# Kernel optimization log

Measured on AMD Instinct MI355X. Metric: run time of the kernel, lower is better.

The kernel has to match this reference:

```python
import jax, jax.numpy as jnp
import numpy as np

D_MODEL = 256
D_FFN = 1024
N_LEVELS = 4
N_HEADS = 8
N_POINTS = 4
HEAD_DIM = D_MODEL // N_HEADS
SPATIAL = [(128, 128), (64, 64), (32, 32), (16, 16)]
LQ = sum(h * w for h, w in SPATIAL)  # 21760
B = 2


def setup_inputs() -> dict:
    key = jax.random.key(0)
    ks = jax.random.split(key, 24)

    def w(k, shape, s=0.02):
        return (jax.random.normal(k, shape) * s).astype(jnp.float32)

    HLP = N_HEADS * N_LEVELS * N_POINTS
    starts = np.cumsum([0] + [h * w_ for h, w_ in SPATIAL[:-1]])
    return {
        "src": jax.random.normal(ks[0], (B, LQ, D_MODEL), jnp.float32),
        "pos": 0.1 * jax.random.normal(ks[1], (B, LQ, D_MODEL), jnp.float32),
        "reference_points": jax.random.uniform(ks[2], (B, LQ, N_LEVELS, 2), jnp.float32),
        "W_off": w(ks[3], (D_MODEL, HLP * 2)),
        "b_off": w(ks[4], (HLP * 2,), 0.5),
        "W_attn": w(ks[5], (D_MODEL, HLP)),
        "b_attn": jnp.zeros((HLP,), jnp.float32),
        "W_val": w(ks[6], (D_MODEL, D_MODEL)),
        "b_val": jnp.zeros((D_MODEL,), jnp.float32),
        "W_out": w(ks[7], (D_MODEL, D_MODEL)),
        "b_out": jnp.zeros((D_MODEL,), jnp.float32),
        "ln1_g": jnp.ones((D_MODEL,), jnp.float32),
        "ln1_b": jnp.zeros((D_MODEL,), jnp.float32),
        "W1": w(ks[8], (D_MODEL, D_FFN)),
        "b1": jnp.zeros((D_FFN,), jnp.float32),
        "W2": w(ks[9], (D_FFN, D_MODEL)),
        "b2": jnp.zeros((D_MODEL,), jnp.float32),
        "ln2_g": jnp.ones((D_MODEL,), jnp.float32),
        "ln2_b": jnp.zeros((D_MODEL,), jnp.float32),
        "spatial_shapes": np.array(SPATIAL, np.int32),
        "level_start_index": np.array(starts, np.int32),
    }


def _layernorm(x, g, b):
    mu = x.mean(-1, keepdims=True)
    var = ((x - mu) ** 2).mean(-1, keepdims=True)
    return (x - mu) * jax.lax.rsqrt(var + 1e-5) * g + b


def _bilinear_sample(v, x, y, H, W):
    # v: [N, H, W, D]; x, y: [N, Lq, P] pixel coords (align_corners=False, zero pad)
    x0f = jnp.floor(x)
    y0f = jnp.floor(y)
    x0 = x0f.astype(jnp.int32)
    y0 = y0f.astype(jnp.int32)
    wx1 = x - x0f
    wy1 = y - y0f
    wx0 = 1.0 - wx1
    wy0 = 1.0 - wy1
    vf = v.reshape(v.shape[0], H * W, v.shape[-1])

    def gather(xi, yi, wt):
        valid = (xi >= 0) & (xi < W) & (yi >= 0) & (yi < H)
        idx = jnp.clip(yi, 0, H - 1) * W + jnp.clip(xi, 0, W - 1)
        g = jnp.take_along_axis(vf, idx.reshape(idx.shape[0], -1)[..., None], axis=1)
        g = g.reshape(*xi.shape, vf.shape[-1])
        return g * (wt * valid.astype(wt.dtype))[..., None]

    return (gather(x0, y0, wx0 * wy0) + gather(x0 + 1, y0, wx1 * wy0)
            + gather(x0, y0 + 1, wx0 * wy1) + gather(x0 + 1, y0 + 1, wx1 * wy1))


def _ms_deform_attn(query, src, reference_points, W_off, b_off, W_attn, b_attn,
                    W_val, b_val, W_out, b_out, spatial_shapes):
    Bq, Lq, _ = query.shape
    ss = np.asarray(spatial_shapes)
    value = (src @ W_val + b_val).reshape(Bq, Lq, N_HEADS, HEAD_DIM)
    off = (query @ W_off + b_off).reshape(Bq, Lq, N_HEADS, N_LEVELS, N_POINTS, 2)
    attn = (query @ W_attn + b_attn).reshape(Bq, Lq, N_HEADS, N_LEVELS * N_POINTS)
    attn = jax.nn.softmax(attn, axis=-1).reshape(Bq, Lq, N_HEADS, N_LEVELS, N_POINTS)
    # offset normalizer = (W, H) per level
    normalizer = jnp.asarray(ss[:, ::-1].astype(np.float32))  # [L, 2]
    loc = reference_points[:, :, None, :, None, :] + off / normalizer[None, None, None, :, None, :]
    # loc: [B, Lq, M, L, P, 2] normalized in [0,1]
    out = jnp.zeros((Bq, N_HEADS, Lq, HEAD_DIM), query.dtype)
    start = 0
    for lvl in range(N_LEVELS):
        H, W = int(ss[lvl, 0]), int(ss[lvl, 1])
        v = value[:, start:start + H * W]                                 # [B, HW, M, D]
        v = v.transpose(0, 2, 1, 3).reshape(Bq * N_HEADS, H, W, HEAD_DIM)
        l = loc[:, :, :, lvl]                                             # [B, Lq, M, P, 2]
        x = (l[..., 0] * W - 0.5).transpose(0, 2, 1, 3).reshape(Bq * N_HEADS, Lq, N_POINTS)
        y = (l[..., 1] * H - 0.5).transpose(0, 2, 1, 3).reshape(Bq * N_HEADS, Lq, N_POINTS)
        sampled = _bilinear_sample(v, x, y, H, W)                         # [BM, Lq, P, D]
        wgt = attn[:, :, :, lvl].transpose(0, 2, 1, 3).reshape(Bq * N_HEADS, Lq, N_POINTS)
        out = out + (sampled * wgt[..., None]).sum(2).reshape(Bq, N_HEADS, Lq, HEAD_DIM)
        start += H * W
    out = out.transpose(0, 2, 1, 3).reshape(Bq, Lq, D_MODEL)
    return out @ W_out + b_out


def reference(src, pos, reference_points, W_off, b_off, W_attn, b_attn, W_val, b_val,
              W_out, b_out, ln1_g, ln1_b, W1, b1, W2, b2, ln2_g, ln2_b,
              spatial_shapes, level_start_index):
    query = src + pos
    src2 = _ms_deform_attn(query, src, reference_points, W_off, b_off, W_attn, b_attn,
                           W_val, b_val, W_out, b_out, spatial_shapes)
    h = _layernorm(src + src2, ln1_g, ln1_b)
    ffn = jax.nn.relu(h @ W1 + b1) @ W2 + b2
    return _layernorm(h + ffn, ln2_g, ln2_b)
```

## Files before the change

kernel.cpp:

```cpp
#include <hip/hip_runtime.h>

typedef __bf16 bf16x8 __attribute__((ext_vector_type(8)));
typedef float f32x4 __attribute__((ext_vector_type(4)));

static constexpr int TOKS = 43520;
static constexpr int LQN  = 21760;

__device__ __forceinline__ unsigned short f2bf(float f) {
  union { float f; unsigned u; } v; v.f = f;
  return (unsigned short)((v.u + 0x7fffu + ((v.u >> 16) & 1u)) >> 16);
}
__device__ __forceinline__ float bf2f(unsigned short b) {
  union { unsigned u; float f; } v; v.u = ((unsigned)b) << 16; return v.f;
}

__global__ __launch_bounds__(256) void prewt_kernel(
    const float* __restrict__ src, const float* __restrict__ pos,
    unsigned short* __restrict__ srcb, unsigned short* __restrict__ qb,
    const float* __restrict__ W_val, const float* __restrict__ W_off,
    const float* __restrict__ W_attn, const float* __restrict__ W_out,
    const float* __restrict__ W1, const float* __restrict__ W2,
    const float* __restrict__ b_off, const float* __restrict__ b_attn,
    unsigned short* __restrict__ Wt_val, unsigned short* __restrict__ Wt_oa,
    unsigned short* __restrict__ Wt_out,
    unsigned short* __restrict__ Wt_1, unsigned short* __restrict__ Wt_2,
    float* __restrict__ b_oa) {
  const int bid = blockIdx.x;
  if (bid < 10880) {
    int i = bid * 256 + threadIdx.x;
    float4 s = ((const float4*)src)[i], p = ((const float4*)pos)[i];
    ((ushort4*)srcb)[i] = make_ushort4(f2bf(s.x), f2bf(s.y), f2bf(s.z), f2bf(s.w));
    ((ushort4*)qb)[i]   = make_ushort4(f2bf(s.x + p.x), f2bf(s.y + p.y),
                                       f2bf(s.z + p.z), f2bf(s.w + p.w));
    return;
  }
  int gid = (bid - 10880) * 256 + threadIdx.x;
  if (gid >= 754048) return;
  if (gid >= 753664) {
    int i = gid - 753664;
    b_oa[i] = (i < 256) ? b_off[i] : b_attn[i - 256];
    return;
  }
  const float* W; unsigned short* Wt; int idx, K, nsh;
  if (gid < 65536)       { W = W_val;  Wt = Wt_val;          idx = gid;          K = 256;  nsh = 8;  }
  else if (gid < 131072) { W = W_off;  Wt = Wt_oa;           idx = gid - 65536;  K = 256;  nsh = 8;  }
  else if (gid < 163840) { W = W_attn; Wt = Wt_oa + 65536;   idx = gid - 131072; K = 256;  nsh = 7;  }
  else if (gid < 229376) { W = W_out;  Wt = Wt_out;          idx = gid - 163840; K = 256;  nsh = 8;  }
  else if (gid < 491520) { W = W1;     Wt = Wt_1;            idx = gid - 229376; K = 256;  nsh = 10; }
  else                   { W = W2;     Wt = Wt_2;            idx = gid - 491520; K = 1024; nsh = 8;  }
  int k = idx >> nsh, n = idx & ((1 << nsh) - 1);
  Wt[n * K + k] = f2bf(W[idx]);
}

template <int K, int OUTOP>
__device__ __forceinline__ void gemm_body(unsigned short* __restrict__ As,
                                          unsigned short* __restrict__ Bs,
                                          const unsigned short* __restrict__ A,
                                          const unsigned short* __restrict__ Bt,
                                          const float* __restrict__ bias,
                                          const unsigned short* __restrict__ res,
                                          unsigned short* __restrict__ Cp,
                                          int N, int bm, int bn) {
  const int t = threadIdx.x;
  const int wave = t >> 6, lane = t & 63;
  const int wm = (wave & 1) << 6, wn = (wave >> 1) << 6;
  const int lr = lane & 15, lq = lane >> 4;
  const int row0 = t >> 2, cb0 = (t & 3) << 3;
  f32x4 acc[4][4] = {};
  const unsigned short* ga = A  + (size_t)(bm * 128 + row0) * K + cb0;
  const unsigned short* gb = Bt + (size_t)(bn * 128 + row0) * K + cb0;
  const size_t gs = (size_t)64 * K;
  uint4 pa0 = *(const uint4*)ga;
  uint4 pa1 = *(const uint4*)(ga + gs);
  uint4 pb0 = *(const uint4*)gb;
  uint4 pb1 = *(const uint4*)(gb + gs);
  int p = 0;
#pragma unroll 1
  for (int k0 = 0; k0 < K; k0 += 32) {
    unsigned short* Ab = As + p * 5120;
    unsigned short* Bb = Bs + p * 5120;
    *(uint4*)&Ab[row0 * 40 + cb0] = pa0;
    *(uint4*)&Ab[(row0 + 64) * 40 + cb0] = pa1;
    *(uint4*)&Bb[row0 * 40 + cb0] = pb0;
    *(uint4*)&Bb[(row0 + 64) * 40 + cb0] = pb1;
    __syncthreads();
    if (k0 + 32 < K) {
      pa0 = *(const uint4*)(ga + k0 + 32);
      pa1 = *(const uint4*)(ga + gs + k0 + 32);
      pb0 = *(const uint4*)(gb + k0 + 32);
      pb1 = *(const uint4*)(gb + gs + k0 + 32);
    }
    bf16x8 af[4], bfr[4];
#pragma unroll
    for (int i = 0; i < 4; i++) af[i] = *(const bf16x8*)&Ab[(wm + i * 16 + lr) * 40 + lq * 8];
#pragma unroll
    for (int j = 0; j < 4; j++) bfr[j] = *(const bf16x8*)&Bb[(wn + j * 16 + lr) * 40 + lq * 8];
#pragma unroll
    for (int i = 0; i < 4; i++)
#pragma unroll
      for (int j = 0; j < 4; j++)
        acc[i][j] = __builtin_amdgcn_mfma_f32_16x16x32_bf16(af[i], bfr[j], acc[i][j], 0, 0, 0);
    p ^= 1;
  }
  const int rb = bm * 128 + wm + lq * 4;
  const int cbase = bn * 128 + wn + lr;
#pragma unroll
  for (int j = 0; j < 4; j++) {
    const int col = cbase + j * 16;
    const float bv = bias[col];
#pragma unroll
    for (int i = 0; i < 4; i++) {
#pragma unroll
      for (int r = 0; r < 4; r++) {
        float v = acc[i][j][r] + bv;
        size_t o = (size_t)(rb + i * 16 + r) * N + col;
        if (OUTOP == 1) Cp[o] = f2bf(v);
        else if (OUTOP == 2) Cp[o] = f2bf(fmaxf(v, 0.f));
        else Cp[o] = f2bf(v + bf2f(res[o]));
      }
    }
  }
}

__global__ __launch_bounds__(256) void proj_kernel(
    const unsigned short* __restrict__ srcb, const unsigned short* __restrict__ qb,
    const unsigned short* __restrict__ Wt_val, const unsigned short* __restrict__ Wt_oa,
    const float* __restrict__ b_val, const float* __restrict__ b_oa,
    unsigned short* __restrict__ valb, unsigned short* __restrict__ oab) {
  __shared__ unsigned short As[2 * 5120];
  __shared__ unsigned short Bs[2 * 5120];
  const int bn = blockIdx.y;
  if (bn < 2)
    gemm_body<256, 1>(As, Bs, srcb, Wt_val, b_val, nullptr, valb, 256, blockIdx.x, bn);
  else
    gemm_body<256, 1>(As, Bs, qb, Wt_oa, b_oa, nullptr, oab, 384, blockIdx.x, bn - 2);
}

template <int K, int MODE>
__device__ __forceinline__ void big_body(unsigned short* __restrict__ As,
                                         unsigned short* __restrict__ Bs,
                                         const unsigned short* __restrict__ A,
                                         const unsigned short* __restrict__ Bt,
                                         const float* __restrict__ bias,
                                         const unsigned short* __restrict__ res,
                                         const float* __restrict__ gamma,
                                         const float* __restrict__ beta,
                                         void* __restrict__ outp,
                                         int N, int bm, int bn) {
  const int t = threadIdx.x;
  const int wave = t >> 6, lane = t & 63;
  const int wm = (wave & 1) << 6, wn = (wave >> 1) << 7;
  const int lr = lane & 15, lq = lane >> 4;
  const int row0 = t >> 2, cb0 = (t & 3) << 3;
  f32x4 acc[4][8] = {};
  const unsigned short* ga = A  + (size_t)(bm * 128 + row0) * K + cb0;
  const unsigned short* gb = Bt + (size_t)(bn * 256 + row0) * K + cb0;
  const size_t gs = (size_t)64 * K;
  uint4 pa0 = *(const uint4*)ga;
  uint4 pa1 = *(const uint4*)(ga + gs);
  uint4 pb0 = *(const uint4*)gb;
  uint4 pb1 = *(const uint4*)(gb + gs);
  uint4 pb2 = *(const uint4*)(gb + 2 * gs);
  uint4 pb3 = *(const uint4*)(gb + 3 * gs);
  int p = 0;
#pragma unroll 1
  for (int k0 = 0; k0 < K; k0 += 32) {
    unsigned short* Ab = As + p * 5120;
    unsigned short* Bb = Bs + p * 10240;
    *(uint4*)&Ab[row0 * 40 + cb0] = pa0;
    *(uint4*)&Ab[(row0 + 64) * 40 + cb0] = pa1;
    *(uint4*)&Bb[row0 * 40 + cb0] = pb0;
    *(uint4*)&Bb[(row0 + 64) * 40 + cb0] = pb1;
    *(uint4*)&Bb[(row0 + 128) * 40 + cb0] = pb2;
    *(uint4*)&Bb[(row0 + 192) * 40 + cb0] = pb3;
    __syncthreads();
    if (k0 + 32 < K) {
      pa0 = *(const uint4*)(ga + k0 + 32);
      pa1 = *(const uint4*)(ga + gs + k0 + 32);
      pb0 = *(const uint4*)(gb + k0 + 32);
      pb1 = *(const uint4*)(gb + gs + k0 + 32);
      pb2 = *(const uint4*)(gb + 2 * gs + k0 + 32);
      pb3 = *(const uint4*)(gb + 3 * gs + k0 + 32);
    }
    bf16x8 af[4], bfr[8];
#pragma unroll
    for (int i = 0; i < 4; i++) af[i]  = *(const bf16x8*)&Ab[(wm + i * 16 + lr) * 40 + lq * 8];
#pragma unroll
    for (int j = 0; j < 8; j++) bfr[j] = *(const bf16x8*)&Bb[(wn + j * 16 + lr) * 40 + lq * 8];
#pragma unroll
    for (int i = 0; i < 4; i++)
#pragma unroll
      for (int j = 0; j < 8; j++)
        acc[i][j] = __builtin_amdgcn_mfma_f32_16x16x32_bf16(af[i], bfr[j], acc[i][j], 0, 0, 0);
    p ^= 1;
  }
  const int rb = bm * 128 + wm + lq * 4;
  if (MODE == 0) {
    const int cbase = bn * 256 + wn + lr;
#pragma unroll
    for (int j = 0; j < 8; j++) {
      const int col = cbase + j * 16;
      const float bv = bias[col];
#pragma unroll
      for (int i = 0; i < 4; i++)
#pragma unroll
        for (int r = 0; r < 4; r++) {
          float v = acc[i][j][r] + bv;
          ((unsigned short*)outp)[(size_t)(rb + i * 16 + r) * N + col] = f2bf(fmaxf(v, 0.f));
        }
    }
    return;
  }
  __syncthreads();
  float* red = (float*)As;
  const int wnIdx = wave >> 1;
  float vsum[4][4], vsq[4][4];
#pragma unroll
  for (int i = 0; i < 4; i++)
#pragma unroll
    for (int r = 0; r < 4; r++) { vsum[i][r] = 0.f; vsq[i][r] = 0.f; }
#pragma unroll
  for (int j = 0; j < 8; j++) {
    const int col = wn + j * 16 + lr;
    const float bv = bias[col];
#pragma unroll
    for (int i = 0; i < 4; i++)
#pragma unroll
      for (int r = 0; r < 4; r++) {
        const int grow = rb + i * 16 + r;
        float v = acc[i][j][r] + bv + bf2f(res[(size_t)grow * 256 + col]);
        acc[i][j][r] = v;
        vsum[i][r] += v;
        vsq[i][r]  += v * v;
      }
  }
#pragma unroll
  for (int m = 1; m <= 8; m <<= 1)
#pragma unroll
    for (int i = 0; i < 4; i++)
#pragma unroll
      for (int r = 0; r < 4; r++) {
        vsum[i][r] += __shfl_xor(vsum[i][r], m, 64);
        vsq[i][r]  += __shfl_xor(vsq[i][r],  m, 64);
      }
  if (lr == 0) {
#pragma unroll
    for (int i = 0; i < 4; i++)
#pragma unroll
      for (int r = 0; r < 4; r++) {
        const int lrow = wm + i * 16 + lq * 4 + r;
        red[wnIdx * 128 + lrow]       = vsum[i][r];
        red[256 + wnIdx * 128 + lrow] = vsq[i][r];
      }
  }
  __syncthreads();
  float mu[4][4], rstd[4][4];
#pragma unroll
  for (int i = 0; i < 4; i++)
#pragma unroll
    for (int r = 0; r < 4; r++) {
      const int lrow = wm + i * 16 + lq * 4 + r;
      const float ts = vsum[i][r] + red[(1 - wnIdx) * 128 + lrow];
      const float tq = vsq[i][r]  + red[256 + (1 - wnIdx) * 128 + lrow];
      const float m_ = ts * (1.f / 256.f);
      float var = tq * (1.f / 256.f) - m_ * m_;
      mu[i][r] = m_;
      rstd[i][r] = rsqrtf(var + 1e-5f);
    }
#pragma unroll
  for (int j = 0; j < 8; j++) {
    const int col = wn + j * 16 + lr;
    const float gg = gamma[col], bb = beta[col];
#pragma unroll
    for (int i = 0; i < 4; i++)
#pragma unroll
      for (int r = 0; r < 4; r++) {
        const int grow = rb + i * 16 + r;
        const float y = (acc[i][j][r] - mu[i][r]) * rstd[i][r] * gg + bb;
        if (MODE == 1) ((unsigned short*)outp)[(size_t)grow * 256 + col] = f2bf(y);
        else           ((float*)outp)[(size_t)grow * 256 + col] = y;
      }
  }
}

__global__ __launch_bounds__(256, 2) void out_ln_kernel(
    const unsigned short* __restrict__ A, const unsigned short* __restrict__ Bt,
    const float* __restrict__ bias, const unsigned short* __restrict__ res,
    const float* __restrict__ gamma, const float* __restrict__ beta,
    unsigned short* __restrict__ C) {
  __shared__ unsigned short As[2 * 5120];
  __shared__ unsigned short Bs[2 * 10240];
  big_body<256, 1>(As, Bs, A, Bt, bias, res, gamma, beta, C, 256, blockIdx.x, 0);
}

__global__ __launch_bounds__(256, 2) void ffn_fused_kernel(
    const unsigned short* __restrict__ h,
    const unsigned short* __restrict__ W1t,
    const unsigned short* __restrict__ W2t,
    const float* __restrict__ b1, const float* __restrict__ b2,
    const float* __restrict__ gamma, const float* __restrict__ beta,
    float* __restrict__ out) {
  __shared__ unsigned short Ah[64 * 264];
  __shared__ unsigned short Hc[64 * 136];
  __shared__ float red[2][4][64];
  const int t = threadIdx.x;
  const int w = t >> 6, lane = t & 63;
  const int lr = lane & 15, lq = lane >> 4;
  const size_t rowbase = (size_t)blockIdx.x * 64;

  {
    const uint4* gsrc = (const uint4*)(h + rowbase * 256);
#pragma unroll
    for (int u = 0; u < 8; u++) {
      const int idx = u * 256 + t;
      const int row = idx >> 5, c8 = idx & 31;
      *(uint4*)&Ah[row * 264 + c8 * 8] = gsrc[idx];
    }
  }
  __syncthreads();

  f32x4 acc2[4][4] = {};
  const int c1base = w * 32;
#pragma unroll 1
  for (int c2 = 0; c2 < 8; c2++) {
    f32x4 acc1[4][2] = {};
    const size_t w1r0 = (size_t)(c2 * 128 + c1base + lr) * 256;
    const size_t w1r1 = (size_t)(c2 * 128 + c1base + 16 + lr) * 256;
    bf16x8 bfn0 = *(const bf16x8*)&W1t[w1r0 + lq * 8];
    bf16x8 bfn1 = *(const bf16x8*)&W1t[w1r1 + lq * 8];
#pragma unroll 1
    for (int ks = 0; ks < 8; ks++) {
      const int k0 = ks * 32;
      bf16x8 b0 = bfn0, b1v = bfn1;
      if (ks < 7) {
        bfn0 = *(const bf16x8*)&W1t[w1r0 + k0 + 32 + lq * 8];
        bfn1 = *(const bf16x8*)&W1t[w1r1 + k0 + 32 + lq * 8];
      }
      bf16x8 af[4];
#pragma unroll
      for (int i = 0; i < 4; i++)
        af[i] = *(const bf16x8*)&Ah[(i * 16 + lr) * 264 + k0 + lq * 8];
#pragma unroll
      for (int i = 0; i < 4; i++) {
        acc1[i][0] = __builtin_amdgcn_mfma_f32_16x16x32_bf16(af[i], b0,  acc1[i][0], 0, 0, 0);
        acc1[i][1] = __builtin_amdgcn_mfma_f32_16x16x32_bf16(af[i], b1v, acc1[i][1], 0, 0, 0);
      }
    }
    __syncthreads();
#pragma unroll
    for (int j = 0; j < 2; j++) {
      const int colc = c1base + j * 16 + lr;
      const float bv = b1[c2 * 128 + colc];
#pragma unroll
      for (int i = 0; i < 4; i++)
#pragma unroll
        for (int r = 0; r < 4; r++)
          Hc[(i * 16 + lq * 4 + r) * 136 + colc] = f2bf(fmaxf(acc1[i][j][r] + bv, 0.f));
    }
    __syncthreads();
    const size_t w2base = (size_t)(w * 64 + lr) * 1024 + c2 * 128;
    bf16x8 cfn0 = *(const bf16x8*)&W2t[w2base + lq * 8];
    bf16x8 cfn1 = *(const bf16x8*)&W2t[w2base + 16 * 1024 + lq * 8];
    bf16x8 cfn2 = *(const bf16x8*)&W2t[w2base + 32 * 1024 + lq * 8];
    bf16x8 cfn3 = *(const bf16x8*)&W2t[w2base + 48 * 1024 + lq * 8];
#pragma unroll 1
    for (int ks = 0; ks < 4; ks++) {
      const int k2 = ks * 32;
      bf16x8 c0 = cfn0, c1 = cfn1, c2v = cfn2, c3 = cfn3;
      if (ks < 3) {
        cfn0 = *(const bf16x8*)&W2t[w2base + k2 + 32 + lq * 8];
        cfn1 = *(const bf16x8*)&W2t[w2base + 16 * 1024 + k2 + 32 + lq * 8];
        cfn2 = *(const bf16x8*)&W2t[w2base + 32 * 1024 + k2 + 32 + lq * 8];
        cfn3 = *(const bf16x8*)&W2t[w2base + 48 * 1024 + k2 + 32 + lq * 8];
      }
      bf16x8 af2[4];
#pragma unroll
      for (int i = 0; i < 4; i++)
        af2[i] = *(const bf16x8*)&Hc[(i * 16 + lr) * 136 + k2 + lq * 8];
#pragma unroll
      for (int i = 0; i < 4; i++) {
        acc2[i][0] = __builtin_amdgcn_mfma_f32_16x16x32_bf16(af2[i], c0,  acc2[i][0], 0, 0, 0);
        acc2[i][1] = __builtin_amdgcn_mfma_f32_16x16x32_bf16(af2[i], c1,  acc2[i][1], 0, 0, 0);
        acc2[i][2] = __builtin_amdgcn_mfma_f32_16x16x32_bf16(af2[i], c2v, acc2[i][2], 0, 0, 0);
        acc2[i][3] = __builtin_amdgcn_mfma_f32_16x16x32_bf16(af2[i], c3,  acc2[i][3], 0, 0, 0);
      }
    }
  }
  float vsum[4][4], vsq[4][4];
#pragma unroll
  for (int i = 0; i < 4; i++)
#pragma unroll
    for (int r = 0; r < 4; r++) { vsum[i][r] = 0.f; vsq[i][r] = 0.f; }
#pragma unroll
  for (int j = 0; j < 4; j++) {
    const int col = w * 64 + j * 16 + lr;
    const float bv = b2[col];
#pragma unroll
    for (int i = 0; i < 4; i++)
#pragma unroll
      for (int r = 0; r < 4; r++) {
        const int row = i * 16 + lq * 4 + r;
        float v = acc2[i][j][r] + bv + bf2f(Ah[row * 264 + col]);
        acc2[i][j][r] = v;
        vsum[i][r] += v;
        vsq[i][r]  += v * v;
      }
  }
#pragma unroll
  for (int m = 1; m <= 8; m <<= 1)
#pragma unroll
    for (int i = 0; i < 4; i++)
#pragma unroll
      for (int r = 0; r < 4; r++) {
        vsum[i][r] += __shfl_xor(vsum[i][r], m, 64);
        vsq[i][r]  += __shfl_xor(vsq[i][r],  m, 64);
      }
  if (lr == 0) {
#pragma unroll
    for (int i = 0; i < 4; i++)
#pragma unroll
      for (int r = 0; r < 4; r++) {
        const int row = i * 16 + lq * 4 + r;
        red[0][w][row] = vsum[i][r];
        red[1][w][row] = vsq[i][r];
      }
  }
  __syncthreads();
  float mu[4][4], rstd[4][4];
#pragma unroll
  for (int i = 0; i < 4; i++)
#pragma unroll
    for (int r = 0; r < 4; r++) {
      const int row = i * 16 + lq * 4 + r;
      const float ts = red[0][0][row] + red[0][1][row] + red[0][2][row] + red[0][3][row];
      const float tq = red[1][0][row] + red[1][1][row] + red[1][2][row] + red[1][3][row];
      const float m_ = ts * (1.f / 256.f);
      mu[i][r] = m_;
      rstd[i][r] = rsqrtf(tq * (1.f / 256.f) - m_ * m_ + 1e-5f);
    }
#pragma unroll
  for (int j = 0; j < 4; j++) {
    const int col = w * 64 + j * 16 + lr;
    const float gg = gamma[col], bb = beta[col];
#pragma unroll
    for (int i = 0; i < 4; i++)
#pragma unroll
      for (int r = 0; r < 4; r++) {
        const int row = i * 16 + lq * 4 + r;
        out[(rowbase + row) * 256 + col] = (acc2[i][j][r] - mu[i][r]) * rstd[i][r] * gg + bb;
      }
  }
}

__device__ __forceinline__ void fma8(uint4 v, float w, float* a) {
  const unsigned uu[4] = {v.x, v.y, v.z, v.w};
#pragma unroll
  for (int i = 0; i < 4; i++) {
    union { unsigned u; float f; } lo, hi;
    lo.u = uu[i] << 16;
    hi.u = uu[i] & 0xffff0000u;
    a[2 * i]     += w * lo.f;
    a[2 * i + 1] += w * hi.f;
  }
}

__global__ __launch_bounds__(256) void deform_kernel(const unsigned short* __restrict__ valb,
                                                     const unsigned short* __restrict__ oab,
                                                     const float* __restrict__ refp,
                                                     unsigned short* __restrict__ outb) {
  __shared__ float4 sW[8][8][17];
  __shared__ int4   sI[8][8][17];
  const int t = threadIdx.x;
  const int bid = blockIdx.x;
  const int nb = (bid & 7) * 680 + (bid >> 3);
  const int tok0 = nb * 8;

  {
    const int g = t >> 5, h = (t >> 2) & 7, l = t & 3;
    const int tok = tok0 + g;
    const unsigned short* lg = oab + (size_t)tok * 384 + 256 + h * 16;
    uint4 lv0 = ((const uint4*)lg)[0];
    uint4 lv1 = ((const uint4*)lg)[1];
    const unsigned lw[8] = {lv0.x, lv0.y, lv0.z, lv0.w, lv1.x, lv1.y, lv1.z, lv1.w};
    float w[16];
#pragma unroll
    for (int i = 0; i < 8; i++) {
      union { unsigned u; float f; } lo, hi;
      lo.u = lw[i] << 16; hi.u = lw[i] & 0xffff0000u;
      w[2 * i] = lo.f; w[2 * i + 1] = hi.f;
    }
    float mx = -1e30f;
#pragma unroll
    for (int i = 0; i < 16; i++) mx = fmaxf(mx, w[i]);
    float s = 0.f;
#pragma unroll
    for (int i = 0; i < 16; i++) { w[i] = __expf(w[i] - mx); s += w[i]; }
    const float inv = 1.f / s;
    uint4 ov = *(const uint4*)(oab + (size_t)tok * 384 + h * 32 + l * 8);
    const unsigned owv[4] = {ov.x, ov.y, ov.z, ov.w};
    float off[8];
#pragma unroll
    for (int i = 0; i < 4; i++) {
      union { unsigned u; float f; } lo, hi;
      lo.u = owv[i] << 16; hi.u = owv[i] & 0xffff0000u;
      off[2 * i] = lo.f; off[2 * i + 1] = hi.f;
    }
    const float* rp = refp + (size_t)tok * 8 + l * 2;
    const int S = 128 >> l;
    const float Sf = (float)S;
    const float rx = rp[0] * Sf - 0.5f;
    const float ry = rp[1] * Sf - 0.5f;
#pragma unroll
    for (int p = 0; p < 4; p++) {
      const int idx = l * 4 + p;
      const float x = rx + off[p * 2 + 0];
      const float y = ry + off[p * 2 + 1];
      const float aw = w[idx] * inv;
      const float x0f = floorf(x), y0f = floorf(y);
      const int x0 = (int)x0f, y0 = (int)y0f;
      const float fx = x - x0f, fy = y - y0f;
      const bool xin0 = (x0 >= 0) & (x0 < S), xin1 = (x0 + 1 >= 0) & (x0 + 1 < S);
      const bool yin0 = (y0 >= 0) & (y0 < S), yin1 = (y0 + 1 >= 0) & (y0 + 1 < S);
      const int xc0 = min(max(x0, 0), S - 1), xc1 = min(max(x0 + 1, 0), S - 1);
      const int yc0 = min(max(y0, 0), S - 1), yc1 = min(max(y0 + 1, 0), S - 1);
      sW[g][h][idx] = make_float4(aw * (1.f - fx) * (1.f - fy) * (float)(xin0 & yin0),
                                  aw * fx * (1.f - fy)         * (float)(xin1 & yin0),
                                  aw * (1.f - fx) * fy         * (float)(xin0 & yin1),
                                  aw * fx * fy                 * (float)(xin1 & yin1));
      sI[g][h][idx] = make_int4((yc0 * S + xc0) << 9, (yc0 * S + xc1) << 9,
                                (yc1 * S + xc0) << 9, (yc1 * S + xc1) << 9);
    }
  }
  __syncthreads();

  const int g = t >> 5, h = (t >> 2) & 7, dc = t & 3;
  const int tok = tok0 + g;
  const int b = tok / LQN;
  float acc[8] = {0.f, 0.f, 0.f, 0.f, 0.f, 0.f, 0.f, 0.f};
  const int ST[4] = {0, 16384, 20480, 21504};
#pragma unroll
  for (int l = 0; l < 4; l++) {
    const char* vbc = (const char*)(valb + ((size_t)(b * LQN + ST[l])) * 256 + h * 32 + dc * 8);
#pragma unroll
    for (int p = 0; p < 4; p++) {
      float4 W4 = sW[g][h][l * 4 + p];
      int4   I4 = sI[g][h][l * 4 + p];
      uint4 v00 = *(const uint4*)(vbc + I4.x);
      uint4 v10 = *(const uint4*)(vbc + I4.y);
      uint4 v01 = *(const uint4*)(vbc + I4.z);
      uint4 v11 = *(const uint4*)(vbc + I4.w);
      fma8(v00, W4.x, acc);
      fma8(v10, W4.y, acc);
      fma8(v01, W4.z, acc);
      fma8(v11, W4.w, acc);
    }
  }
  unsigned o[4];
#pragma unroll
  for (int i = 0; i < 4; i++)
    o[i] = (unsigned)f2bf(acc[2 * i]) | ((unsigned)f2bf(acc[2 * i + 1]) << 16);
  *(uint4*)(outb + (size_t)tok * 256 + h * 32 + dc * 8) = make_uint4(o[0], o[1], o[2], o[3]);
}

extern "C" void kernel_launch(void* const* d_in, const int* in_sizes, int n_in,
                              void* d_out, int out_size, void* d_ws, size_t ws_size,
                              hipStream_t stream) {
  (void)in_sizes; (void)n_in; (void)out_size; (void)ws_size;
  const float* src    = (const float*)d_in[0];
  const float* pos    = (const float*)d_in[1];
  const float* refp   = (const float*)d_in[2];
  const float* W_off  = (const float*)d_in[3];
  const float* b_off  = (const float*)d_in[4];
  const float* W_attn = (const float*)d_in[5];
  const float* b_attn = (const float*)d_in[6];
  const float* W_val  = (const float*)d_in[7];
  const float* b_val  = (const float*)d_in[8];
  const float* W_out  = (const float*)d_in[9];
  const float* b_out  = (const float*)d_in[10];
  const float* ln1_g  = (const float*)d_in[11];
  const float* ln1_b  = (const float*)d_in[12];
  const float* W1     = (const float*)d_in[13];
  const float* b1     = (const float*)d_in[14];
  const float* W2     = (const float*)d_in[15];
  const float* b2     = (const float*)d_in[16];
  const float* ln2_g  = (const float*)d_in[17];
  const float* ln2_b  = (const float*)d_in[18];

  char* ws = (char*)d_ws;
  unsigned short* Wt_val = (unsigned short*)ws;
  unsigned short* Wt_oa  = Wt_val + 65536;
  unsigned short* Wt_out = Wt_oa + 98304;
  unsigned short* Wt_1   = Wt_out + 65536;
  unsigned short* Wt_2   = Wt_1 + 262144;
  float*          b_oa   = (float*)(Wt_2 + 262144);
  const size_t WPOOL = 2u * 1024 * 1024;

  const size_t SZ_bf = (size_t)TOKS * 256 * 2;
  const size_t SZ_oa = (size_t)TOKS * 384 * 2;

  unsigned short* srcb = (unsigned short*)(ws + WPOOL);
  unsigned short* qb   = (unsigned short*)(ws + WPOOL + SZ_bf);
  unsigned short* valb = (unsigned short*)(ws + WPOOL + 2 * SZ_bf);
  unsigned short* oab  = (unsigned short*)(ws + WPOOL + 3 * SZ_bf);
  unsigned short* h_bf = (unsigned short*)(ws + WPOOL + 3 * SZ_bf + SZ_oa);
  unsigned short* attnoutb = qb;

  prewt_kernel<<<13826, 256, 0, stream>>>(src, pos, srcb, qb,
                                          W_val, W_off, W_attn, W_out, W1, W2, b_off, b_attn,
                                          Wt_val, Wt_oa, Wt_out, Wt_1, Wt_2, b_oa);

  proj_kernel<<<dim3(340, 5), 256, 0, stream>>>(srcb, qb, Wt_val, Wt_oa, b_val, b_oa,
                                                valb, oab);

  deform_kernel<<<TOKS / 8, 256, 0, stream>>>(valb, oab, refp, attnoutb);

  out_ln_kernel<<<340, 256, 0, stream>>>(attnoutb, Wt_out, b_out, srcb, ln1_g, ln1_b, h_bf);

  ffn_fused_kernel<<<680, 256, 0, stream>>>(h_bf, Wt_1, Wt_2, b1, b2, ln2_g, ln2_b,
                                            (float*)d_out);
}
```

Baseline: 435.6 us.

## Fuse output projection and first LayerNorm into the FFN kernel

Merges the out-projection GEMM, residual add and LayerNorm1 into the fused FFN kernel, so each 64-row block computes h in shared memory and feeds it straight into the FFN. This drops one kernel launch and the bf16 round trip of h through global memory. In exchange, the out-projection now runs with 64-row tiles that read W_out straight from global memory rather than the previous 128x256 LDS-tiled GEMM. A barrier is added before the reuse of the reduction buffer.

New measurement: 432.0 us. Within noise of the previous version (-0.8%).

```diff
diff --git a/kernel.cpp b/kernel.cpp
--- a/kernel.cpp
+++ b/kernel.cpp
@@ -136,169 +136,16 @@
     gemm_body<256, 1>(As, Bs, qb, Wt_oa, b_oa, nullptr, oab, 384, blockIdx.x, bn - 2);
 }
 
-template <int K, int MODE>
-__device__ __forceinline__ void big_body(unsigned short* __restrict__ As,
-                                         unsigned short* __restrict__ Bs,
-                                         const unsigned short* __restrict__ A,
-                                         const unsigned short* __restrict__ Bt,
-                                         const float* __restrict__ bias,
-                                         const unsigned short* __restrict__ res,
-                                         const float* __restrict__ gamma,
-                                         const float* __restrict__ beta,
-                                         void* __restrict__ outp,
-                                         int N, int bm, int bn) {
-  const int t = threadIdx.x;
-  const int wave = t >> 6, lane = t & 63;
-  const int wm = (wave & 1) << 6, wn = (wave >> 1) << 7;
-  const int lr = lane & 15, lq = lane >> 4;
-  const int row0 = t >> 2, cb0 = (t & 3) << 3;
-  f32x4 acc[4][8] = {};
-  const unsigned short* ga = A  + (size_t)(bm * 128 + row0) * K + cb0;
-  const unsigned short* gb = Bt + (size_t)(bn * 256 + row0) * K + cb0;
-  const size_t gs = (size_t)64 * K;
-  uint4 pa0 = *(const uint4*)ga;
-  uint4 pa1 = *(const uint4*)(ga + gs);
-  uint4 pb0 = *(const uint4*)gb;
-  uint4 pb1 = *(const uint4*)(gb + gs);
-  uint4 pb2 = *(const uint4*)(gb + 2 * gs);
-  uint4 pb3 = *(const uint4*)(gb + 3 * gs);
-  int p = 0;
-#pragma unroll 1
-  for (int k0 = 0; k0 < K; k0 += 32) {
-    unsigned short* Ab = As + p * 5120;
-    unsigned short* Bb = Bs + p * 10240;
-    *(uint4*)&Ab[row0 * 40 + cb0] = pa0;
-    *(uint4*)&Ab[(row0 + 64) * 40 + cb0] = pa1;
-    *(uint4*)&Bb[row0 * 40 + cb0] = pb0;
-    *(uint4*)&Bb[(row0 + 64) * 40 + cb0] = pb1;
-    *(uint4*)&Bb[(row0 + 128) * 40 + cb0] = pb2;
-    *(uint4*)&Bb[(row0 + 192) * 40 + cb0] = pb3;
-    __syncthreads();
-    if (k0 + 32 < K) {
-      pa0 = *(const uint4*)(ga + k0 + 32);
-      pa1 = *(const uint4*)(ga + gs + k0 + 32);
-      pb0 = *(const uint4*)(gb + k0 + 32);
-      pb1 = *(const uint4*)(gb + gs + k0 + 32);
-      pb2 = *(const uint4*)(gb + 2 * gs + k0 + 32);
-      pb3 = *(const uint4*)(gb + 3 * gs + k0 + 32);
-    }
-    bf16x8 af[4], bfr[8];
-#pragma unroll
-    for (int i = 0; i < 4; i++) af[i]  = *(const bf16x8*)&Ab[(wm + i * 16 + lr) * 40 + lq * 8];
-#pragma unroll
-    for (int j = 0; j < 8; j++) bfr[j] = *(const bf16x8*)&Bb[(wn + j * 16 + lr) * 40 + lq * 8];
-#pragma unroll
-    for (int i = 0; i < 4; i++)
-#pragma unroll
-      for (int j = 0; j < 8; j++)
-        acc[i][j] = __builtin_amdgcn_mfma_f32_16x16x32_bf16(af[i], bfr[j], acc[i][j], 0, 0, 0);
-    p ^= 1;
-  }
-  const int rb = bm * 128 + wm + lq * 4;
-  if (MODE == 0) {
-    const int cbase = bn * 256 + wn + lr;
-#pragma unroll
-    for (int j = 0; j < 8; j++) {
-      const int col = cbase + j * 16;
-      const float bv = bias[col];
-#pragma unroll
-      for (int i = 0; i < 4; i++)
-#pragma unroll
-        for (int r = 0; r < 4; r++) {
-          float v = acc[i][j][r] + bv;
-          ((unsigned short*)outp)[(size_t)(rb + i * 16 + r) * N + col] = f2bf(fmaxf(v, 0.f));
-        }
-    }
-    return;
-  }
-  __syncthreads();
-  float* red = (float*)As;
-  const int wnIdx = wave >> 1;
-  float vsum[4][4], vsq[4][4];
-#pragma unroll
-  for (int i = 0; i < 4; i++)
-#pragma unroll
-    for (int r = 0; r < 4; r++) { vsum[i][r] = 0.f; vsq[i][r] = 0.f; }
-#pragma unroll
-  for (int j = 0; j < 8; j++) {
-    const int col = wn + j * 16 + lr;
-    const float bv = bias[col];
-#pragma unroll
-    for (int i = 0; i < 4; i++)
-#pragma unroll
-      for (int r = 0; r < 4; r++) {
-        const int grow = rb + i * 16 + r;
-        float v = acc[i][j][r] + bv + bf2f(res[(size_t)grow * 256 + col]);
-        acc[i][j][r] = v;
-        vsum[i][r] += v;
-        vsq[i][r]  += v * v;
-      }
-  }
-#pragma unroll
-  for (int m = 1; m <= 8; m <<= 1)
-#pragma unroll
-    for (int i = 0; i < 4; i++)
-#pragma unroll
-      for (int r = 0; r < 4; r++) {
-        vsum[i][r] += __shfl_xor(vsum[i][r], m, 64);
-        vsq[i][r]  += __shfl_xor(vsq[i][r],  m, 64);
-      }
-  if (lr == 0) {
-#pragma unroll
-    for (int i = 0; i < 4; i++)
-#pragma unroll
-      for (int r = 0; r < 4; r++) {
-        const int lrow = wm + i * 16 + lq * 4 + r;
-        red[wnIdx * 128 + lrow]       = vsum[i][r];
-        red[256 + wnIdx * 128 + lrow] = vsq[i][r];
-      }
-  }
-  __syncthreads();
-  float mu[4][4], rstd[4][4];
-#pragma unroll
-  for (int i = 0; i < 4; i++)
-#pragma unroll
-    for (int r = 0; r < 4; r++) {
-      const int lrow = wm + i * 16 + lq * 4 + r;
-      const float ts = vsum[i][r] + red[(1 - wnIdx) * 128 + lrow];
-      const float tq = vsq[i][r]  + red[256 + (1 - wnIdx) * 128 + lrow];
-      const float m_ = ts * (1.f / 256.f);
-      float var = tq * (1.f / 256.f) - m_ * m_;
-      mu[i][r] = m_;
-      rstd[i][r] = rsqrtf(var + 1e-5f);
-    }
-#pragma unroll
-  for (int j = 0; j < 8; j++) {
-    const int col = wn + j * 16 + lr;
-    const float gg = gamma[col], bb = beta[col];
-#pragma unroll
-    for (int i = 0; i < 4; i++)
-#pragma unroll
-      for (int r = 0; r < 4; r++) {
-        const int grow = rb + i * 16 + r;
-        const float y = (acc[i][j][r] - mu[i][r]) * rstd[i][r] * gg + bb;
-        if (MODE == 1) ((unsigned short*)outp)[(size_t)grow * 256 + col] = f2bf(y);
-        else           ((float*)outp)[(size_t)grow * 256 + col] = y;
-      }
-  }
-}
-
-__global__ __launch_bounds__(256, 2) void out_ln_kernel(
-    const unsigned short* __restrict__ A, const unsigned short* __restrict__ Bt,
-    const float* __restrict__ bias, const unsigned short* __restrict__ res,
-    const float* __restrict__ gamma, const float* __restrict__ beta,
-    unsigned short* __restrict__ C) {
-  __shared__ unsigned short As[2 * 5120];
-  __shared__ unsigned short Bs[2 * 10240];
-  big_body<256, 1>(As, Bs, A, Bt, bias, res, gamma, beta, C, 256, blockIdx.x, 0);
-}
-
-__global__ __launch_bounds__(256, 2) void ffn_fused_kernel(
-    const unsigned short* __restrict__ h,
+__global__ __launch_bounds__(256, 2) void fused_tail_kernel(
+    const unsigned short* __restrict__ attn,
+    const unsigned short* __restrict__ Wot,
+    const float* __restrict__ b_out,
+    const unsigned short* __restrict__ srcres,
+    const float* __restrict__ g1, const float* __restrict__ be1,
     const unsigned short* __restrict__ W1t,
     const unsigned short* __restrict__ W2t,
     const float* __restrict__ b1, const float* __restrict__ b2,
-    const float* __restrict__ gamma, const float* __restrict__ beta,
+    const float* __restrict__ g2, const float* __restrict__ be2,
     float* __restrict__ out) {
   __shared__ unsigned short Ah[64 * 264];
   __shared__ unsigned short Hc[64 * 136];
@@ -309,12 +156,111 @@
   const size_t rowbase = (size_t)blockIdx.x * 64;
 
   {
-    const uint4* gsrc = (const uint4*)(h + rowbase * 256);
+    const uint4* gsrc = (const uint4*)(attn + rowbase * 256);
 #pragma unroll
     for (int u = 0; u < 8; u++) {
       const int idx = u * 256 + t;
       const int row = idx >> 5, c8 = idx & 31;
       *(uint4*)&Ah[row * 264 + c8 * 8] = gsrc[idx];
+    }
+  }
+  __syncthreads();
+
+  f32x4 acc0[4][4] = {};
+  {
+    const size_t wb = (size_t)(w * 64 + lr) * 256;
+    bf16x8 pf0 = *(const bf16x8*)&Wot[wb + lq * 8];
+    bf16x8 pf1 = *(const bf16x8*)&Wot[wb + 16 * 256 + lq * 8];
+    bf16x8 pf2 = *(const bf16x8*)&Wot[wb + 32 * 256 + lq * 8];
+    bf16x8 pf3 = *(const bf16x8*)&Wot[wb + 48 * 256 + lq * 8];
+#pragma unroll 1
+    for (int ks = 0; ks < 8; ks++) {
+      const int k0 = ks * 32;
+      bf16x8 c0 = pf0, c1 = pf1, c2 = pf2, c3 = pf3;
+      if (ks < 7) {
+        pf0 = *(const bf16x8*)&Wot[wb + k0 + 32 + lq * 8];
+        pf1 = *(const bf16x8*)&Wot[wb + 16 * 256 + k0 + 32 + lq * 8];
+        pf2 = *(const bf16x8*)&Wot[wb + 32 * 256 + k0 + 32 + lq * 8];
+        pf3 = *(const bf16x8*)&Wot[wb + 48 * 256 + k0 + 32 + lq * 8];
+      }
+      bf16x8 af[4];
+#pragma unroll
+      for (int i = 0; i < 4; i++)
+        af[i] = *(const bf16x8*)&Ah[(i * 16 + lr) * 264 + k0 + lq * 8];
+#pragma unroll
+      for (int i = 0; i < 4; i++) {
+        acc0[i][0] = __builtin_amdgcn_mfma_f32_16x16x32_bf16(af[i], c0, acc0[i][0], 0, 0, 0);
+        acc0[i][1] = __builtin_amdgcn_mfma_f32_16x16x32_bf16(af[i], c1, acc0[i][1], 0, 0, 0);
+        acc0[i][2] = __builtin_amdgcn_mfma_f32_16x16x32_bf16(af[i], c2, acc0[i][2], 0, 0, 0);
+        acc0[i][3] = __builtin_amdgcn_mfma_f32_16x16x32_bf16(af[i], c3, acc0[i][3], 0, 0, 0);
+      }
+    }
+  }
+  {
+    float vsum[4][4], vsq[4][4];
+#pragma unroll
+    for (int i = 0; i < 4; i++)
+#pragma unroll
+      for (int r = 0; r < 4; r++) { vsum[i][r] = 0.f; vsq[i][r] = 0.f; }
+#pragma unroll
+    for (int j = 0; j < 4; j++) {
+      const int col = w * 64 + j * 16 + lr;
+      const float bv = b_out[col];
+#pragma unroll
+      for (int i = 0; i < 4; i++)
+#pragma unroll
+        for (int r = 0; r < 4; r++) {
+          const int row = i * 16 + lq * 4 + r;
+          float v = acc0[i][j][r] + bv + bf2f(srcres[(rowbase + row) * 256 + col]);
+          acc0[i][j][r] = v;
+          vsum[i][r] += v;
+          vsq[i][r]  += v * v;
+        }
+    }
+#pragma unroll
+    for (int m = 1; m <= 8; m <<= 1)
+#pragma unroll
+      for (int i = 0; i < 4; i++)
+#pragma unroll
+        for (int r = 0; r < 4; r++) {
+          vsum[i][r] += __shfl_xor(vsum[i][r], m, 64);
+          vsq[i][r]  += __shfl_xor(vsq[i][r],  m, 64);
+        }
+    if (lr == 0) {
+#pragma unroll
+      for (int i = 0; i < 4; i++)
+#pragma unroll
+        for (int r = 0; r < 4; r++) {
+          const int row = i * 16 + lq * 4 + r;
+          red[0][w][row] = vsum[i][r];
+          red[1][w][row] = vsq[i][r];
+        }
+    }
+    __syncthreads();
+    float mu[4][4], rstd[4][4];
+#pragma unroll
+    for (int i = 0; i < 4; i++)
+#pragma unroll
+      for (int r = 0; r < 4; r++) {
+        const int row = i * 16 + lq * 4 + r;
+        const float ts = red[0][0][row] + red[0][1][row] + red[0][2][row] + red[0][3][row];
+        const float tq = red[1][0][row] + red[1][1][row] + red[1][2][row] + red[1][3][row];
+        const float m_ = ts * (1.f / 256.f);
+        mu[i][r] = m_;
+        rstd[i][r] = rsqrtf(tq * (1.f / 256.f) - m_ * m_ + 1e-5f);
+      }
+#pragma unroll
+    for (int j = 0; j < 4; j++) {
+      const int col = w * 64 + j * 16 + lr;
+      const float gg = g1[col], bb = be1[col];
+#pragma unroll
+      for (int i = 0; i < 4; i++)
+#pragma unroll
+        for (int r = 0; r < 4; r++) {
+          const int row = i * 16 + lq * 4 + r;
+          const float y = (acc0[i][j][r] - mu[i][r]) * rstd[i][r] * gg + bb;
+          Ah[row * 264 + col] = f2bf(y);
+        }
     }
   }
   __syncthreads();
@@ -415,6 +361,7 @@
         vsum[i][r] += __shfl_xor(vsum[i][r], m, 64);
         vsq[i][r]  += __shfl_xor(vsq[i][r],  m, 64);
       }
+  __syncthreads();
   if (lr == 0) {
 #pragma unroll
     for (int i = 0; i < 4; i++)
@@ -441,7 +388,7 @@
 #pragma unroll
   for (int j = 0; j < 4; j++) {
     const int col = w * 64 + j * 16 + lr;
-    const float gg = gamma[col], bb = beta[col];
+    const float gg = g2[col], bb = be2[col];
 #pragma unroll
     for (int i = 0; i < 4; i++)
 #pragma unroll
@@ -602,7 +549,6 @@
   unsigned short* qb   = (unsigned short*)(ws + WPOOL + SZ_bf);
   unsigned short* valb = (unsigned short*)(ws + WPOOL + 2 * SZ_bf);
   unsigned short* oab  = (unsigned short*)(ws + WPOOL + 3 * SZ_bf);
-  unsigned short* h_bf = (unsigned short*)(ws + WPOOL + 3 * SZ_bf + SZ_oa);
   unsigned short* attnoutb = qb;
 
   prewt_kernel<<<13826, 256, 0, stream>>>(src, pos, srcb, qb,
@@ -614,8 +560,7 @@
 
   deform_kernel<<<TOKS / 8, 256, 0, stream>>>(valb, oab, refp, attnoutb);
 
-  out_ln_kernel<<<340, 256, 0, stream>>>(attnoutb, Wt_out, b_out, srcb, ln1_g, ln1_b, h_bf);
-
-  ffn_fused_kernel<<<680, 256, 0, stream>>>(h_bf, Wt_1, Wt_2, b1, b2, ln2_g, ln2_b,
-                                            (float*)d_out);
-}
+  fused_tail_kernel<<<680, 256, 0, stream>>>(attnoutb, Wt_out, b_out, srcb, ln1_g, ln1_b,
+                                             Wt_1, Wt_2, b1, b2, ln2_g, ln2_b,
+                                             (float*)d_out);
+}
```
